# Optimization experiments

Hardware: AMD Instinct MI355X
Metric: run time of the kernel (lower is better)

## Reference

```python
import jax, jax.numpy as jnp
import numpy as np

N_NODES = 100000


def gat_conv(x, edge_index, W, att_src, att_dst, bias, concat=True, negative_slope=0.2):
    """PyG-style GATConv (eval mode, dropout off, self-loops added)."""
    N = x.shape[0]
    H, C = att_src.shape
    # add self loops (PyG default add_self_loops=True)
    ar = jnp.arange(N, dtype=edge_index.dtype)
    ei = jnp.concatenate([edge_index, jnp.stack([ar, ar])], axis=1)
    src, dst = ei[0], ei[1]

    h = (x @ W).reshape(N, H, C)                       # [N,H,C]
    a_src = (h * att_src[None]).sum(-1)                # [N,H]
    a_dst = (h * att_dst[None]).sum(-1)                # [N,H]

    e = jax.nn.leaky_relu(a_src[src] + a_dst[dst], negative_slope)  # [E,H]
    # segment softmax over destination nodes
    e_max = jax.ops.segment_max(e, dst, num_segments=N)            # [N,H]
    ex = jnp.exp(e - jax.lax.stop_gradient(e_max)[dst])
    denom = jax.ops.segment_sum(ex, dst, num_segments=N)           # [N,H]
    alpha = ex / (denom[dst] + 1e-16)                              # [E,H]

    out = jax.ops.segment_sum(alpha[:, :, None] * h[src], dst, num_segments=N)  # [N,H,C]
    out = out.reshape(N, H * C) if concat else out.mean(axis=1)
    return out + bias


def setup_inputs() -> dict:
    key = jax.random.key(0)
    ks = jax.random.split(key, 9)
    N, E, F_in, H, C = N_NODES, 3200000, 16, 4, 8
    x = jax.random.normal(ks[0], (N, F_in), dtype=jnp.float32)
    edge_index = jax.random.randint(ks[1], (2, E), 0, N, dtype=jnp.int64)
    s1 = 1.0 / np.sqrt(F_in)
    s2 = 1.0 / np.sqrt(H * C)
    return {
        "x": x,
        "edge_index": edge_index,
        "W1": jax.random.normal(ks[2], (F_in, H * C), dtype=jnp.float32) * s1,
        "att_src1": jax.random.normal(ks[3], (H, C), dtype=jnp.float32) * s2,
        "att_dst1": jax.random.normal(ks[4], (H, C), dtype=jnp.float32) * s2,
        "b1": jnp.zeros((H * C,), dtype=jnp.float32),
        "W2": jax.random.normal(ks[5], (H * C, 1), dtype=jnp.float32) * s2,
        "att_src2": jax.random.normal(ks[6], (1, 1), dtype=jnp.float32),
        "att_dst2": jax.random.normal(ks[7], (1, 1), dtype=jnp.float32),
        "b2": jnp.zeros((1,), dtype=jnp.float32),
    }


def reference(x, edge_index, W1, att_src1, att_dst1, b1, W2, att_src2, att_dst2, b2):
    h = jax.nn.elu(gat_conv(x, edge_index, W1, att_src1, att_dst1, b1, concat=True))
    return gat_conv(h, edge_index, W2, att_src2, att_dst2, b2, concat=False)
```

## Files before the change

kernel.cpp:

```cpp
#include <hip/hip_runtime.h>
#include <hip/hip_fp8.h>

#define LRELU_SLOPE 0.2f
#define BN 64
#define BSH 6
#define NC 2048
#define CAP 3840
#define TILE 16384

__device__ __forceinline__ float lrelu(float x) { return x > 0.f ? x : LRELU_SLOPE * x; }
__device__ __forceinline__ float eexp(float x)  { return __expf(fminf(x, 80.f)); }

__device__ __forceinline__ unsigned short f2bf(float f) {
    unsigned u = __float_as_uint(f);
    u += 0x7FFF + ((u >> 16) & 1);
    return (unsigned short)(u >> 16);
}
__device__ __forceinline__ float bf2f(unsigned short h) {
    return __uint_as_float((unsigned)h << 16);
}

typedef float fx2 __attribute__((ext_vector_type(2)));

#if __has_builtin(__builtin_amdgcn_cvt_pk_f32_fp8) && __has_builtin(__builtin_amdgcn_cvt_pk_fp8_f32)
#define HW_FP8 1
#else
#define HW_FP8 0
#endif

__device__ __forceinline__ void fp8x8_to_f32(uint2 r, float* o) {
#if HW_FP8
    fx2 a = __builtin_amdgcn_cvt_pk_f32_fp8((int)r.x, false);
    fx2 b = __builtin_amdgcn_cvt_pk_f32_fp8((int)r.x, true);
    fx2 c = __builtin_amdgcn_cvt_pk_f32_fp8((int)r.y, false);
    fx2 d = __builtin_amdgcn_cvt_pk_f32_fp8((int)r.y, true);
    o[0]=a.x; o[1]=a.y; o[2]=b.x; o[3]=b.y;
    o[4]=c.x; o[5]=c.y; o[6]=d.x; o[7]=d.y;
#else
#pragma unroll
    for (int i = 0; i < 8; ++i) {
        unsigned bb = (i < 4 ? r.x : r.y) >> ((i & 3) * 8);
        unsigned em = bb & 0x7F;
        float f = (em >= 8) ? __uint_as_float((em << 20) + 0x3C000000u)
                            : (float)em * 0.001953125f;
        o[i] = (bb & 0x80) ? -f : f;
    }
#endif
}

__device__ __forceinline__ unsigned f32x4_to_fp8(float a, float b, float c, float d) {
#if HW_FP8
    int w = __builtin_amdgcn_cvt_pk_fp8_f32(a, b, 0, false);
    w = __builtin_amdgcn_cvt_pk_fp8_f32(c, d, w, true);
    return (unsigned)w;
#else
    __hip_fp8_e4m3 qa(a), qb(b), qc(c), qd(d);
    return (unsigned)qa.__x | ((unsigned)qb.__x << 8) |
           ((unsigned)qc.__x << 16) | ((unsigned)qd.__x << 24);
#endif
}

__global__ __launch_bounds__(256) void kA(
    const float* __restrict__ x, const float* __restrict__ W1,
    const float* __restrict__ att_src1, const float* __restrict__ att_dst1,
    unsigned char* __restrict__ h1, unsigned short* __restrict__ as1,
    float* __restrict__ ad1,
    const int* __restrict__ dst, int* __restrict__ hist, int* __restrict__ bukcnt,
    int N, int E, int nbn)
{
    __shared__ float sW[512];
    __shared__ float sAs[32], sAd[32];
    __shared__ int hl[NC];
    int tid = threadIdx.x;

    if ((int)blockIdx.x >= nbn) {
        int blk = blockIdx.x - nbn;
        for (int i = tid; i < NC; i += 256) hl[i] = 0;
        __syncthreads();
        int e0 = blk * TILE, e1 = min(e0 + TILE, E);
        for (int e = e0 + tid; e < e1; e += 256)
            atomicAdd(&hl[dst[e] >> BSH], 1);
        __syncthreads();
        for (int i = tid; i < NC; i += 256) {
            int v = hl[i];
            hist[(size_t)blk * NC + i] = v;
            if (v) atomicAdd(bukcnt + i, v);
        }
        return;
    }

    for (int i = tid; i < 512; i += 256) sW[i] = W1[i];
    if (tid < 32) { sAs[tid] = att_src1[tid]; sAd[tid] = att_dst1[tid]; }
    __syncthreads();
    int n = blockIdx.x * 256 + tid;
    if (n >= N) return;

    float xr[16];
    const float4* xp = (const float4*)(x + (size_t)n * 16);
    float4 v0 = xp[0], v1 = xp[1], v2 = xp[2], v3 = xp[3];
    xr[0]=v0.x; xr[1]=v0.y; xr[2]=v0.z;  xr[3]=v0.w;
    xr[4]=v1.x; xr[5]=v1.y; xr[6]=v1.z;  xr[7]=v1.w;
    xr[8]=v2.x; xr[9]=v2.y; xr[10]=v2.z; xr[11]=v2.w;
    xr[12]=v3.x;xr[13]=v3.y;xr[14]=v3.z; xr[15]=v3.w;

    float h[32];
#pragma unroll
    for (int j = 0; j < 32; ++j) {
        float acc = 0.f;
#pragma unroll
        for (int i = 0; i < 16; ++i) acc = fmaf(xr[i], sW[i * 32 + j], acc);
        h[j] = acc;
    }

    float asr[4], adr[4];
#pragma unroll
    for (int hh = 0; hh < 4; ++hh) {
        float as = 0.f, ad = 0.f;
#pragma unroll
        for (int c = 0; c < 8; ++c) {
            as = fmaf(h[hh * 8 + c], sAs[hh * 8 + c], as);
            ad = fmaf(h[hh * 8 + c], sAd[hh * 8 + c], ad);
        }
        asr[hh] = as; adr[hh] = ad;
    }

    unsigned q[8];
#pragma unroll
    for (int j = 0; j < 8; ++j)
        q[j] = f32x4_to_fp8(h[4*j], h[4*j+1], h[4*j+2], h[4*j+3]);
    uint4* hp = (uint4*)(h1 + (size_t)n * 32);
    hp[0] = make_uint4(q[0], q[1], q[2], q[3]);
    hp[1] = make_uint4(q[4], q[5], q[6], q[7]);

    ushort4 aq;
    aq.x = f2bf(asr[0]); aq.y = f2bf(asr[1]); aq.z = f2bf(asr[2]); aq.w = f2bf(asr[3]);
    *(ushort4*)(as1 + (size_t)n * 4) = aq;
    *(float4*)(ad1 + (size_t)n * 4) = make_float4(adr[0], adr[1], adr[2], adr[3]);
}

__global__ __launch_bounds__(256) void kscan(
    const int* __restrict__ hist, int* __restrict__ histoff,
    const int* __restrict__ bukcnt, int* __restrict__ bukoff, int NBLK)
{
    __shared__ int sm[256 * 17];
    int tid = threadIdx.x;
    if ((int)blockIdx.x == NC / 16) {
        __shared__ int sd[256];
        int4 a = ((const int4*)bukcnt)[2 * tid];
        int4 c = ((const int4*)bukcnt)[2 * tid + 1];
        int tsum = a.x + a.y + a.z + a.w + c.x + c.y + c.z + c.w;
        sd[tid] = tsum; __syncthreads();
        for (int off = 1; off < 256; off <<= 1) {
            int t = (tid >= off) ? sd[tid - off] : 0; __syncthreads();
            sd[tid] += t; __syncthreads();
        }
        int excl = sd[tid] - tsum;
        int4 oa, ob;
        oa.x = excl;        oa.y = oa.x + a.x; oa.z = oa.y + a.y; oa.w = oa.z + a.z;
        ob.x = oa.w + a.w;  ob.y = ob.x + c.x; ob.z = ob.y + c.y; ob.w = ob.z + c.z;
        ((int4*)bukoff)[2 * tid] = oa;
        ((int4*)bukoff)[2 * tid + 1] = ob;
        return;
    }
    int c0 = blockIdx.x * 16;
    int v[16], own[16];
    if (tid < NBLK) {
        const int4* rp = (const int4*)(hist + (size_t)tid * NC + c0);
        int4 a = rp[0], b = rp[1], c = rp[2], d = rp[3];
        v[0]=a.x; v[1]=a.y; v[2]=a.z;  v[3]=a.w;
        v[4]=b.x; v[5]=b.y; v[6]=b.z;  v[7]=b.w;
        v[8]=c.x; v[9]=c.y; v[10]=c.z; v[11]=c.w;
        v[12]=d.x; v[13]=d.y; v[14]=d.z; v[15]=d.w;
    } else {
#pragma unroll
        for (int i = 0; i < 16; ++i) v[i] = 0;
    }
#pragma unroll
    for (int i = 0; i < 16; ++i) own[i] = v[i];

    int* myrow = sm + tid * 17;
#pragma unroll
    for (int i = 0; i < 16; ++i) myrow[i] = v[i];
    __syncthreads();
    for (int off = 1; off < 256; off <<= 1) {
        int t[16];
        if (tid >= off) {
            const int* nb = sm + (tid - off) * 17;
#pragma unroll
            for (int i = 0; i < 16; ++i) t[i] = nb[i];
        } else {
#pragma unroll
            for (int i = 0; i < 16; ++i) t[i] = 0;
        }
        __syncthreads();
#pragma unroll
        for (int i = 0; i < 16; ++i) { v[i] += t[i]; myrow[i] = v[i]; }
        __syncthreads();
    }
    if (tid < NBLK) {
        int4* wp = (int4*)(histoff + (size_t)tid * NC + c0);
        int e[16];
#pragma unroll
        for (int i = 0; i < 16; ++i) e[i] = v[i] - own[i];
        wp[0] = make_int4(e[0], e[1], e[2], e[3]);
        wp[1] = make_int4(e[4], e[5], e[6], e[7]);
        wp[2] = make_int4(e[8], e[9], e[10], e[11]);
        wp[3] = make_int4(e[12], e[13], e[14], e[15]);
    }
}

__global__ __launch_bounds__(1024) void kpass2(
    const int* __restrict__ src, const int* __restrict__ dst,
    const int* __restrict__ hist, const int* __restrict__ histoff,
    const int* __restrict__ bukoff,
    unsigned* __restrict__ ebuk, int E)
{
    __shared__ unsigned staged[TILE];
    __shared__ int bstart[NC + 1];
    __shared__ int cur[NC];
    __shared__ int partial[1024];
    int tid = threadIdx.x, blk = blockIdx.x;

    int2 c2 = ((const int2*)(hist + (size_t)blk * NC))[tid];
    int tsum = c2.x + c2.y;
    partial[tid] = tsum;
    __syncthreads();
    for (int off = 1; off < 1024; off <<= 1) {
        int t = (tid >= off) ? partial[tid - off] : 0; __syncthreads();
        partial[tid] += t; __syncthreads();
    }
    int excl = partial[tid] - tsum;
    bstart[2 * tid] = excl; bstart[2 * tid + 1] = excl + c2.x;
    cur[2 * tid] = excl;    cur[2 * tid + 1] = excl + c2.x;
    if (tid == 1023) bstart[NC] = excl + c2.x + c2.y;
    __syncthreads();

    int e0 = blk * TILE, e1 = min(e0 + TILE, E);
    for (int e = e0 + tid; e < e1; e += 1024) {
        int s = src[e], d = dst[e];
        int b = d >> BSH;
        int pos = atomicAdd(&cur[b], 1);
        staged[pos] = ((unsigned)(d & (BN - 1)) << 17) | (unsigned)s;
    }
    __syncthreads();

    for (int b = tid; b < NC; b += 1024) {
        int p0 = bstart[b], p1 = bstart[b + 1];
        int gb = bukoff[b] + histoff[(size_t)blk * NC + b];
        for (int p = p0; p < p1; ++p)
            ebuk[gb + (p - p0)] = staged[p];
    }
}

__global__ __launch_bounds__(256, 6) void ksort_agg1(
    unsigned* __restrict__ ebuk, const int* __restrict__ bukoff,
    const unsigned char* __restrict__ h1, const unsigned short* __restrict__ as1,
    const float* __restrict__ ad1,
    const float* __restrict__ b1, const float* __restrict__ W2,
    float* __restrict__ h2, int* __restrict__ rowptr, int N)
{
    __shared__ int sbuf[CAP];
    __shared__ int cnt[BN], exc[BN], cur[BN];
    __shared__ float sb[32], sw[32];
    int tid = threadIdx.x;
    int b = blockIdx.x;
    int n0 = b << BSH;
    int r0 = bukoff[b], r1 = bukoff[b + 1];
    int tot = r1 - r0;

    if (tid < 32) { sb[tid] = b1[tid]; sw[tid] = W2[tid]; }
    if (tid < BN) cnt[tid] = 0;
    __syncthreads();

    for (int i = tid; i < tot; i += 256)
        atomicAdd(&cnt[ebuk[r0 + i] >> 17], 1);
    __syncthreads();

    if (tid < BN) exc[tid] = cnt[tid];
    __syncthreads();
    for (int off = 1; off < BN; off <<= 1) {
        int t = 0;
        if (tid < BN && tid >= off) t = exc[tid - off];
        __syncthreads();
        if (tid < BN) exc[tid] += t;
        __syncthreads();
    }
    if (tid < BN) {
        int e = exc[tid] - cnt[tid];
        exc[tid] = e;
        cur[tid] = e;
        int n = n0 + tid;
        if (n <= N) rowptr[n] = r0 + e;
    }
    __syncthreads();

    for (int i = tid; i < tot; i += 256) {
        unsigned pk = ebuk[r0 + i];
        int dl = pk >> 17;
        int pos = atomicAdd(&cur[dl], 1);
        if (pos < CAP) sbuf[pos] = (int)(pk & 0x1FFFF);
    }
    __syncthreads();
    for (int i = tid; i < tot; i += 256)
        ebuk[r0 + i] = (unsigned)sbuf[min(i, CAP - 1)];

    int g = tid >> 2, l = tid & 3;
    {
        int dl = g;
        int n = n0 + dl;
        if (n < N) {
            float adh = ad1[(size_t)n * 4 + l];
            float ass = bf2f(as1[(size_t)n * 4 + l]);
            float wself = eexp(lrelu(ass + adh));
            float dsum = wself;
            float acc[8], hv[8];
            fp8x8_to_f32(*(const uint2*)(h1 + (size_t)n * 32 + l * 8), hv);
#pragma unroll
            for (int ch = 0; ch < 8; ++ch) acc[ch] = wself * hv[ch];

            int p0 = exc[dl];
            int p1 = min(p0 + cnt[dl], CAP);
            int p = p0;
            for (; p + 4 <= p1; p += 4) {
                int sidx[4];
                float av[4];
                uint2 uv[4];
#pragma unroll
                for (int q = 0; q < 4; ++q) sidx[q] = sbuf[p + q];
#pragma unroll
                for (int q = 0; q < 4; ++q) {
                    av[q] = bf2f(as1[(size_t)sidx[q] * 4 + l]);
                    uv[q] = *(const uint2*)(h1 + (size_t)sidx[q] * 32 + l * 8);
                }
#pragma unroll
                for (int q = 0; q < 4; ++q) {
                    float w = eexp(lrelu(av[q] + adh));
                    float sv[8];
                    fp8x8_to_f32(uv[q], sv);
                    dsum += w;
#pragma unroll
                    for (int ch = 0; ch < 8; ++ch)
                        acc[ch] = fmaf(w, sv[ch], acc[ch]);
                }
            }
            for (; p < p1; ++p) {
                int s = sbuf[p];
                float ash = bf2f(as1[(size_t)s * 4 + l]);
                float sv[8];
                fp8x8_to_f32(*(const uint2*)(h1 + (size_t)s * 32 + l * 8), sv);
                float w = eexp(lrelu(ash + adh));
                dsum += w;
#pragma unroll
                for (int ch = 0; ch < 8; ++ch)
                    acc[ch] = fmaf(w, sv[ch], acc[ch]);
            }
            float inv = 1.f / (dsum + 1e-16f);
            float partial = 0.f;
#pragma unroll
            for (int ch = 0; ch < 8; ++ch) {
                float o = fmaf(acc[ch], inv, sb[l * 8 + ch]);
                o = o > 0.f ? o : __expf(o) - 1.f;
                partial = fmaf(o, sw[l * 8 + ch], partial);
            }
            partial += __shfl_xor(partial, 1);
            partial += __shfl_xor(partial, 2);
            if (l == 0) h2[n] = partial;
        }
    }
}

__global__ __launch_bounds__(256) void kagg2(
    const unsigned* __restrict__ esrc, const int* __restrict__ rowptr,
    const float* __restrict__ h2,
    const float* __restrict__ att_src2, const float* __restrict__ att_dst2,
    const float* __restrict__ b2, float* __restrict__ out, int N)
{
    int tid = threadIdx.x;
    int g = tid >> 3, l = tid & 7;
    int n = blockIdx.x * 32 + g;
    if (n >= N) return;
    float s2 = att_src2[0], d2 = att_dst2[0];
    int r0 = rowptr[n], r1 = rowptr[n + 1];
    float h2d = h2[n];
    float add = h2d * d2;
    float den = 0.f, acc = 0.f;
    if (l == 0) {
        float ws = eexp(lrelu(fmaf(h2d, s2, add)));
        den = ws; acc = ws * h2d;
    }
    for (int p = r0 + l; p < r1; p += 8) {
        int s = (int)esrc[p];
        float hs = h2[s];
        float w = eexp(lrelu(fmaf(hs, s2, add)));
        den += w;
        acc = fmaf(w, hs, acc);
    }
    den += __shfl_xor(den, 1); acc += __shfl_xor(acc, 1);
    den += __shfl_xor(den, 2); acc += __shfl_xor(acc, 2);
    den += __shfl_xor(den, 4); acc += __shfl_xor(acc, 4);
    if (l == 0) out[n] = acc / (den + 1e-16f) + b2[0];
}

extern "C" void kernel_launch(void* const* d_in, const int* in_sizes, int n_in,
                              void* d_out, int out_size, void* d_ws, size_t ws_size,
                              hipStream_t stream)
{
    const float* x        = (const float*)d_in[0];
    const int*   ei       = (const int*)d_in[1];
    const float* W1       = (const float*)d_in[2];
    const float* att_src1 = (const float*)d_in[3];
    const float* att_dst1 = (const float*)d_in[4];
    const float* b1       = (const float*)d_in[5];
    const float* W2       = (const float*)d_in[6];
    const float* att_src2 = (const float*)d_in[7];
    const float* att_dst2 = (const float*)d_in[8];
    const float* b2       = (const float*)d_in[9];

    const int N = in_sizes[0] / 16;
    const int E = in_sizes[1] / 2;
    const int* src = ei;
    const int* dst = ei + E;

    const int NBUK = (N + BN - 1) >> BSH;
    const int NBLK = (E + TILE - 1) / TILE;
    const int nb_n = (N + 255) / 256;

    unsigned char* h1   = (unsigned char*)d_ws;
    unsigned short* as1 = (unsigned short*)(h1 + (size_t)N * 32);
    float* ad1   = (float*)(as1 + (size_t)N * 4);
    float* h2    = ad1 + (size_t)N * 4;
    int* rowptr  = (int*)(h2 + N);
    int* bukcnt  = rowptr + N + 64;
    int* bukoff  = bukcnt + NC;
    int* hist    = bukoff + NC;
    int* histoff = hist + (size_t)NBLK * NC;
    unsigned* ebuk = (unsigned*)(histoff + (size_t)NBLK * NC);

    hipMemsetAsync(bukcnt, 0, NC * sizeof(int), stream);

    kA<<<nb_n + NBLK, 256, 0, stream>>>(x, W1, att_src1, att_dst1,
                                        h1, as1, ad1, dst, hist, bukcnt,
                                        N, E, nb_n);
    kscan<<<NC / 16 + 1, 256, 0, stream>>>(hist, histoff, bukcnt, bukoff, NBLK);
    kpass2<<<NBLK, 1024, 0, stream>>>(src, dst, hist, histoff, bukoff, ebuk, E);
    ksort_agg1<<<NBUK, 256, 0, stream>>>(ebuk, bukoff, h1, as1, ad1,
                                         b1, W2, h2, rowptr, N);
    kagg2<<<(N + 31) / 32, 256, 0, stream>>>(ebuk, rowptr, h2,
                                             att_src2, att_dst2,
                                             b2, (float*)d_out, N);
}
```

Before: 196.6 us.

## Halve edge tile size, chunk block scan, drop atomics, and unroll aggregation loops

Halves the edge tile so kpass2 runs twice as many 512-thread blocks with a smaller LDS footprint (16-bit bucket starts, one aliased shared buffer). The histogram scan now loops over block chunks with a carry and writes bucket totals directly, which removes the global bucket-count atomics and the memset. A separate single-block kernel then does the bucket-offset scan. The layer-1 gather unroll goes from 4 to 8 and the layer-2 aggregation is unrolled by 2, to raise memory-level parallelism at the cost of an extra launch, more hist traffic and more registers.

Result: no change. 194.7 us (-1.0%).

```diff
diff --git a/kernel.cpp b/kernel.cpp
--- a/kernel.cpp
+++ b/kernel.cpp
@@ -6,7 +6,7 @@
 #define BSH 6
 #define NC 2048
 #define CAP 3840
-#define TILE 16384
+#define TILE 8192
 
 __device__ __forceinline__ float lrelu(float x) { return x > 0.f ? x : LRELU_SLOPE * x; }
 __device__ __forceinline__ float eexp(float x)  { return __expf(fminf(x, 80.f)); }
@@ -65,7 +65,7 @@
     const float* __restrict__ att_src1, const float* __restrict__ att_dst1,
     unsigned char* __restrict__ h1, unsigned short* __restrict__ as1,
     float* __restrict__ ad1,
-    const int* __restrict__ dst, int* __restrict__ hist, int* __restrict__ bukcnt,
+    const int* __restrict__ dst, int* __restrict__ hist,
     int N, int E, int nbn)
 {
     __shared__ float sW[512];
@@ -81,11 +81,8 @@
         for (int e = e0 + tid; e < e1; e += 256)
             atomicAdd(&hl[dst[e] >> BSH], 1);
         __syncthreads();
-        for (int i = tid; i < NC; i += 256) {
-            int v = hl[i];
-            hist[(size_t)blk * NC + i] = v;
-            if (v) atomicAdd(bukcnt + i, v);
-        }
+        for (int i = tid; i < NC; i += 256)
+            hist[(size_t)blk * NC + i] = hl[i];
         return;
     }
 
@@ -140,103 +137,131 @@
 
 __global__ __launch_bounds__(256) void kscan(
     const int* __restrict__ hist, int* __restrict__ histoff,
-    const int* __restrict__ bukcnt, int* __restrict__ bukoff, int NBLK)
+    int* __restrict__ bukcnt, int NBLK)
 {
     __shared__ int sm[256 * 17];
     int tid = threadIdx.x;
-    if ((int)blockIdx.x == NC / 16) {
-        __shared__ int sd[256];
-        int4 a = ((const int4*)bukcnt)[2 * tid];
-        int4 c = ((const int4*)bukcnt)[2 * tid + 1];
-        int tsum = a.x + a.y + a.z + a.w + c.x + c.y + c.z + c.w;
-        sd[tid] = tsum; __syncthreads();
+    int c0 = blockIdx.x * 16;
+    int carry[16];
+#pragma unroll
+    for (int i = 0; i < 16; ++i) carry[i] = 0;
+    int* myrow = sm + tid * 17;
+
+    for (int base = 0; base < NBLK; base += 256) {
+        int idx = base + tid;
+        int v[16], own[16];
+        if (idx < NBLK) {
+            const int4* rp = (const int4*)(hist + (size_t)idx * NC + c0);
+            int4 a = rp[0], b = rp[1], c = rp[2], d = rp[3];
+            v[0]=a.x; v[1]=a.y; v[2]=a.z;  v[3]=a.w;
+            v[4]=b.x; v[5]=b.y; v[6]=b.z;  v[7]=b.w;
+            v[8]=c.x; v[9]=c.y; v[10]=c.z; v[11]=c.w;
+            v[12]=d.x; v[13]=d.y; v[14]=d.z; v[15]=d.w;
+        } else {
+#pragma unroll
+            for (int i = 0; i < 16; ++i) v[i] = 0;
+        }
+#pragma unroll
+        for (int i = 0; i < 16; ++i) { own[i] = v[i]; myrow[i] = v[i]; }
+        __syncthreads();
         for (int off = 1; off < 256; off <<= 1) {
-            int t = (tid >= off) ? sd[tid - off] : 0; __syncthreads();
-            sd[tid] += t; __syncthreads();
+            int t[16];
+            if (tid >= off) {
+                const int* nb = sm + (tid - off) * 17;
+#pragma unroll
+                for (int i = 0; i < 16; ++i) t[i] = nb[i];
+            } else {
+#pragma unroll
+                for (int i = 0; i < 16; ++i) t[i] = 0;
+            }
+            __syncthreads();
+#pragma unroll
+            for (int i = 0; i < 16; ++i) { v[i] += t[i]; myrow[i] = v[i]; }
+            __syncthreads();
         }
-        int excl = sd[tid] - tsum;
-        int4 oa, ob;
-        oa.x = excl;        oa.y = oa.x + a.x; oa.z = oa.y + a.y; oa.w = oa.z + a.z;
-        ob.x = oa.w + a.w;  ob.y = ob.x + c.x; ob.z = ob.y + c.y; ob.w = ob.z + c.z;
-        ((int4*)bukoff)[2 * tid] = oa;
-        ((int4*)bukoff)[2 * tid + 1] = ob;
-        return;
-    }
-    int c0 = blockIdx.x * 16;
-    int v[16], own[16];
-    if (tid < NBLK) {
-        const int4* rp = (const int4*)(hist + (size_t)tid * NC + c0);
-        int4 a = rp[0], b = rp[1], c = rp[2], d = rp[3];
-        v[0]=a.x; v[1]=a.y; v[2]=a.z;  v[3]=a.w;
-        v[4]=b.x; v[5]=b.y; v[6]=b.z;  v[7]=b.w;
-        v[8]=c.x; v[9]=c.y; v[10]=c.z; v[11]=c.w;
-        v[12]=d.x; v[13]=d.y; v[14]=d.z; v[15]=d.w;
-    } else {
-#pragma unroll
-        for (int i = 0; i < 16; ++i) v[i] = 0;
-    }
-#pragma unroll
-    for (int i = 0; i < 16; ++i) own[i] = v[i];
-
-    int* myrow = sm + tid * 17;
-#pragma unroll
-    for (int i = 0; i < 16; ++i) myrow[i] = v[i];
-    __syncthreads();
+        if (idx < NBLK) {
+            int4* wp = (int4*)(histoff + (size_t)idx * NC + c0);
+            int e[16];
+#pragma unroll
+            for (int i = 0; i < 16; ++i) e[i] = carry[i] + v[i] - own[i];
+            wp[0] = make_int4(e[0], e[1], e[2], e[3]);
+            wp[1] = make_int4(e[4], e[5], e[6], e[7]);
+            wp[2] = make_int4(e[8], e[9], e[10], e[11]);
+            wp[3] = make_int4(e[12], e[13], e[14], e[15]);
+        }
+        const int* last = sm + 255 * 17;
+#pragma unroll
+        for (int i = 0; i < 16; ++i) carry[i] += last[i];
+        __syncthreads();
+    }
+    if (tid == 0) {
+        int4* bp = (int4*)(bukcnt + c0);
+        bp[0] = make_int4(carry[0], carry[1], carry[2], carry[3]);
+        bp[1] = make_int4(carry[4], carry[5], carry[6], carry[7]);
+        bp[2] = make_int4(carry[8], carry[9], carry[10], carry[11]);
+        bp[3] = make_int4(carry[12], carry[13], carry[14], carry[15]);
+    }
+}
+
+__global__ __launch_bounds__(256) void kscanB(
+    const int* __restrict__ bukcnt, int* __restrict__ bukoff)
+{
+    __shared__ int sd[256];
+    int tid = threadIdx.x;
+    int4 a = ((const int4*)bukcnt)[2 * tid];
+    int4 c = ((const int4*)bukcnt)[2 * tid + 1];
+    int tsum = a.x + a.y + a.z + a.w + c.x + c.y + c.z + c.w;
+    sd[tid] = tsum; __syncthreads();
     for (int off = 1; off < 256; off <<= 1) {
-        int t[16];
-        if (tid >= off) {
-            const int* nb = sm + (tid - off) * 17;
-#pragma unroll
-            for (int i = 0; i < 16; ++i) t[i] = nb[i];
-        } else {
-#pragma unroll
-            for (int i = 0; i < 16; ++i) t[i] = 0;
-        }
-        __syncthreads();
-#pragma unroll
-        for (int i = 0; i < 16; ++i) { v[i] += t[i]; myrow[i] = v[i]; }
-        __syncthreads();
-    }
-    if (tid < NBLK) {
-        int4* wp = (int4*)(histoff + (size_t)tid * NC + c0);
-        int e[16];
-#pragma unroll
-        for (int i = 0; i < 16; ++i) e[i] = v[i] - own[i];
-        wp[0] = make_int4(e[0], e[1], e[2], e[3]);
-        wp[1] = make_int4(e[4], e[5], e[6], e[7]);
-        wp[2] = make_int4(e[8], e[9], e[10], e[11]);
-        wp[3] = make_int4(e[12], e[13], e[14], e[15]);
-    }
-}
-
-__global__ __launch_bounds__(1024) void kpass2(
+        int t = (tid >= off) ? sd[tid - off] : 0; __syncthreads();
+        sd[tid] += t; __syncthreads();
+    }
+    int excl = sd[tid] - tsum;
+    int4 oa, ob;
+    oa.x = excl;        oa.y = oa.x + a.x; oa.z = oa.y + a.y; oa.w = oa.z + a.z;
+    ob.x = oa.w + a.w;  ob.y = ob.x + c.x; ob.z = ob.y + c.y; ob.w = ob.z + c.z;
+    ((int4*)bukoff)[2 * tid] = oa;
+    ((int4*)bukoff)[2 * tid + 1] = ob;
+}
+
+#define KP2_BST (TILE * 4)
+#define KP2_CUR (KP2_BST + ((NC + 1) * 2 + 2))
+#define KP2_LDS (KP2_CUR + NC * 4)
+
+__global__ __launch_bounds__(512) void kpass2(
     const int* __restrict__ src, const int* __restrict__ dst,
     const int* __restrict__ hist, const int* __restrict__ histoff,
     const int* __restrict__ bukoff,
     unsigned* __restrict__ ebuk, int E)
 {
-    __shared__ unsigned staged[TILE];
-    __shared__ int bstart[NC + 1];
-    __shared__ int cur[NC];
-    __shared__ int partial[1024];
+    __shared__ __align__(16) unsigned char smem[KP2_LDS];
+    unsigned* staged = (unsigned*)smem;
+    unsigned short* bstart = (unsigned short*)(smem + KP2_BST);
+    int* cur = (int*)(smem + KP2_CUR);
+    int* partial = (int*)smem;
+
     int tid = threadIdx.x, blk = blockIdx.x;
-
-    int2 c2 = ((const int2*)(hist + (size_t)blk * NC))[tid];
-    int tsum = c2.x + c2.y;
+    int4 c4 = ((const int4*)(hist + (size_t)blk * NC))[tid];
+    int tsum = c4.x + c4.y + c4.z + c4.w;
     partial[tid] = tsum;
     __syncthreads();
-    for (int off = 1; off < 1024; off <<= 1) {
+    for (int off = 1; off < 512; off <<= 1) {
         int t = (tid >= off) ? partial[tid - off] : 0; __syncthreads();
         partial[tid] += t; __syncthreads();
     }
     int excl = partial[tid] - tsum;
-    bstart[2 * tid] = excl; bstart[2 * tid + 1] = excl + c2.x;
-    cur[2 * tid] = excl;    cur[2 * tid + 1] = excl + c2.x;
-    if (tid == 1023) bstart[NC] = excl + c2.x + c2.y;
+    int b4 = tid * 4;
+    int e0v = excl, e1v = excl + c4.x, e2v = e1v + c4.y, e3v = e2v + c4.z;
+    cur[b4] = e0v; cur[b4+1] = e1v; cur[b4+2] = e2v; cur[b4+3] = e3v;
+    bstart[b4]   = (unsigned short)e0v;
+    bstart[b4+1] = (unsigned short)e1v;
+    bstart[b4+2] = (unsigned short)e2v;
+    bstart[b4+3] = (unsigned short)e3v;
+    if (tid == 511) bstart[NC] = (unsigned short)(e3v + c4.w);
     __syncthreads();
 
     int e0 = blk * TILE, e1 = min(e0 + TILE, E);
-    for (int e = e0 + tid; e < e1; e += 1024) {
+    for (int e = e0 + tid; e < e1; e += 512) {
         int s = src[e], d = dst[e];
         int b = d >> BSH;
         int pos = atomicAdd(&cur[b], 1);
@@ -244,7 +269,7 @@
     }
     __syncthreads();
 
-    for (int b = tid; b < NC; b += 1024) {
+    for (int b = tid; b < NC; b += 512) {
         int p0 = bstart[b], p1 = bstart[b + 1];
         int gb = bukoff[b] + histoff[(size_t)blk * NC + b];
         for (int p = p0; p < p1; ++p)
@@ -321,19 +346,19 @@
             int p0 = exc[dl];
             int p1 = min(p0 + cnt[dl], CAP);
             int p = p0;
-            for (; p + 4 <= p1; p += 4) {
-                int sidx[4];
-                float av[4];
-                uint2 uv[4];
-#pragma unroll
-                for (int q = 0; q < 4; ++q) sidx[q] = sbuf[p + q];
-#pragma unroll
-                for (int q = 0; q < 4; ++q) {
+            for (; p + 8 <= p1; p += 8) {
+                int sidx[8];
+                float av[8];
+                uint2 uv[8];
+#pragma unroll
+                for (int q = 0; q < 8; ++q) sidx[q] = sbuf[p + q];
+#pragma unroll
+                for (int q = 0; q < 8; ++q) {
                     av[q] = bf2f(as1[(size_t)sidx[q] * 4 + l]);
                     uv[q] = *(const uint2*)(h1 + (size_t)sidx[q] * 32 + l * 8);
                 }
 #pragma unroll
-                for (int q = 0; q < 4; ++q) {
+                for (int q = 0; q < 8; ++q) {
                     float w = eexp(lrelu(av[q] + adh));
                     float sv[8];
                     fp8x8_to_f32(uv[q], sv);
@@ -388,7 +413,17 @@
         float ws = eexp(lrelu(fmaf(h2d, s2, add)));
         den = ws; acc = ws * h2d;
     }
-    for (int p = r0 + l; p < r1; p += 8) {
+    int p = r0 + l;
+    for (; p + 8 < r1; p += 16) {
+        int s0 = (int)esrc[p], s1 = (int)esrc[p + 8];
+        float ha = h2[s0], hb = h2[s1];
+        float wa = eexp(lrelu(fmaf(ha, s2, add)));
+        float wb = eexp(lrelu(fmaf(hb, s2, add)));
+        den += wa + wb;
+        acc = fmaf(wa, ha, acc);
+        acc = fmaf(wb, hb, acc);
+    }
+    if (p < r1) {
         int s = (int)esrc[p];
         float hs = h2[s];
         float w = eexp(lrelu(fmaf(hs, s2, add)));
@@ -436,13 +471,12 @@
     int* histoff = hist + (size_t)NBLK * NC;
     unsigned* ebuk = (unsigned*)(histoff + (size_t)NBLK * NC);
 
-    hipMemsetAsync(bukcnt, 0, NC * sizeof(int), stream);
-
     kA<<<nb_n + NBLK, 256, 0, stream>>>(x, W1, att_src1, att_dst1,
-                                        h1, as1, ad1, dst, hist, bukcnt,
+                                        h1, as1, ad1, dst, hist,
                                         N, E, nb_n);
-    kscan<<<NC / 16 + 1, 256, 0, stream>>>(hist, histoff, bukcnt, bukoff, NBLK);
-    kpass2<<<NBLK, 1024, 0, stream>>>(src, dst, hist, histoff, bukoff, ebuk, E);
+    kscan<<<NC / 16, 256, 0, stream>>>(hist, histoff, bukcnt, NBLK);
+    kscanB<<<1, 256, 0, stream>>>(bukcnt, bukoff);
+    kpass2<<<NBLK, 512, 0, stream>>>(src, dst, hist, histoff, bukoff, ebuk, E);
     ksort_agg1<<<NBUK, 256, 0, stream>>>(ebuk, bukoff, h1, as1, ad1,
                                          b1, W2, h2, rowptr, N);
     kagg2<<<(N + 31) / 32, 256, 0, stream>>>(ebuk, rowptr, h2,
```
